# Performance work log

Measured on AMD Instinct MI355X. Metric: run time of the kernel, lower is better.

Reference implementation:

```python
import jax, jax.numpy as jnp
import numpy as np
import math

DIM = 147      # input feature dim
EMB = 64       # in_dim * head_cnt
M = 32         # int(EMB * kernel_ratio)
EPS_LN = 1e-5
EPS = 1e-8


def layer_norm(x, g, b, eps=EPS_LN):
    mu = jnp.mean(x, axis=-1, keepdims=True)
    var = jnp.mean(jnp.square(x - mu), axis=-1, keepdims=True)
    return (x - mu) * jax.lax.rsqrt(var + eps) * g + b


def prm_exp(x, W_rf):
    # x: [b, t, e], W_rf: [m, e]
    xd = 0.5 * jnp.sum(x * x, axis=-1, keepdims=True)        # [b, t, 1]
    wtx = jnp.einsum('bte,me->btm', x, W_rf)                  # [b, t, m]
    return jnp.exp(wtx - xd) / math.sqrt(M)


def setup_inputs() -> dict:
    key = jax.random.key(0)
    ks = jax.random.split(key, 16)
    B, T = 32, 3136
    s_in = 1.0 / math.sqrt(DIM)
    s_emb = 1.0 / math.sqrt(EMB)
    inp = {
        'x':      jax.random.normal(ks[0], (B, T, DIM), jnp.float32),
        'w_kqv':  jax.random.uniform(ks[1], (3 * EMB, DIM), jnp.float32, -s_in, s_in),
        'b_kqv':  jax.random.uniform(ks[2], (3 * EMB,), jnp.float32, -s_in, s_in),
        'w_proj': jax.random.uniform(ks[3], (EMB, EMB), jnp.float32, -s_emb, s_emb),
        'b_proj': jax.random.uniform(ks[4], (EMB,), jnp.float32, -s_emb, s_emb),
        'g1':     jnp.ones((DIM,), jnp.float32),
        'beta1':  jnp.zeros((DIM,), jnp.float32),
        'g2':     jnp.ones((EMB,), jnp.float32),
        'beta2':  jnp.zeros((EMB,), jnp.float32),
        'w_m1':   jax.random.uniform(ks[5], (EMB, EMB), jnp.float32, -s_emb, s_emb),
        'b_m1':   jax.random.uniform(ks[6], (EMB,), jnp.float32, -s_emb, s_emb),
        'w_m2':   jax.random.uniform(ks[7], (EMB, EMB), jnp.float32, -s_emb, s_emb),
        'b_m2':   jax.random.uniform(ks[8], (EMB,), jnp.float32, -s_emb, s_emb),
        # orthogonal random-feature matrix scaled by sqrt(m) (buffer 'w')
        'W_rf':   jnp.asarray(np.linalg.qr(np.random.RandomState(0).randn(EMB, EMB))[0][:M] * math.sqrt(M), jnp.float32),
    }
    return inp


def reference(x, w_kqv, b_kqv, w_proj, b_proj, g1, beta1, g2, beta2,
              w_m1, b_m1, w_m2, b_m2, W_rf):
    # --- single_attn(norm1(x)) ---
    xn = layer_norm(x, g1, beta1)
    kqv = xn @ w_kqv.T + b_kqv                                  # [b, t, 3e]
    k, q, v = jnp.split(kqv, 3, axis=-1)
    kp = prm_exp(k, W_rf)                                       # [b, t, m]
    qp = prm_exp(q, W_rf)                                       # [b, t, m]
    D = jnp.einsum('btm,bm->bt', qp, kp.sum(axis=1))[..., None]  # [b, t, 1]
    kptv = jnp.einsum('bte,btm->bem', v, kp)                    # [b, e, m]
    y = jnp.einsum('btm,bem->bte', qp, kptv) / (D + EPS)        # [b, t, e]
    y = v + (y @ w_proj.T + b_proj)                             # residual on v
    # --- y + mlp(norm2(y)) ---
    yn = layer_norm(y, g2, beta2)
    h = jax.nn.gelu(yn @ w_m1.T + b_m1, approximate=False)
    out = y + (h @ w_m2.T + b_m2)
    return out
```

## Files before the change

### kernel.cpp

```cpp
#include <hip/hip_runtime.h>
#include <hip/hip_bf16.h>

#define BB 32
#define TT 3136
#define DD 147
#define EE 64
#define MM 32
#define BT (BB*TT)

typedef __hip_bfloat16 bf16;
typedef __attribute__((ext_vector_type(8))) short s8v;
typedef __attribute__((ext_vector_type(4))) float f4v;

__device__ __forceinline__ float b2f(bf16 v){ return __bfloat162float(v); }
__device__ __forceinline__ bf16 f2b(float v){ return __float2bfloat16(v); }
__device__ __forceinline__ unsigned pack2(float a, float b){
  union { bf16 h[2]; unsigned u; } cv; cv.h[0]=f2b(a); cv.h[1]=f2b(b); return cv.u;
}

template<typename T>
__device__ __forceinline__ float cvt1(T v);
template<> __device__ __forceinline__ float cvt1<float>(float v){ return v; }
template<> __device__ __forceinline__ float cvt1<bf16>(bf16 v){ return __bfloat162float(v); }

__device__ __forceinline__ int bf16flag(const void* g1){
  return (*(const unsigned*)g1 == 0x3F803F80u) ? 1 : 0;
}

template<typename T>
__device__ void cvt_body(int idx,
    const T* wkqv, const T* bkqv, const T* Wrf, const T* wproj, const T* bproj,
    const T* g2, const T* be2, const T* wm1, const T* bm1, const T* wm2,
    const T* bm2, const T* g1, const T* be1,
    bf16* Bprep, bf16* WrfB, bf16* w0B, float* bprojF,
    float* g2F, float* be2F, bf16* w1B, float* bm1F, bf16* w2B,
    float* bm2F, float* c2F)
{
  if (idx < 30720){
    int n = idx/160, k = idx - n*160;
    Bprep[idx] = f2b(k < DD ? cvt1(wkqv[n*DD + k]) * cvt1(g1[k]) : 0.f);
    return;
  }
  idx -= 30720;
  if (idx < 2048){ WrfB[idx] = f2b(cvt1(Wrf[idx])); return; }
  idx -= 2048;
  if (idx < 4608){
    int e = idx/72, c = idx - e*72;
    w0B[idx] = f2b(c < 64 ? cvt1(wproj[e*64 + c]) : 0.f); return;
  }
  idx -= 4608;
  if (idx < 64){ bprojF[idx] = cvt1(bproj[idx]); return; }
  idx -= 64;
  if (idx < 64){ g2F[idx] = cvt1(g2[idx]); return; }
  idx -= 64;
  if (idx < 64){ be2F[idx] = cvt1(be2[idx]); return; }
  idx -= 64;
  if (idx < 4608){
    int e = idx/72, c = idx - e*72;
    w1B[idx] = f2b(c < 64 ? cvt1(wm1[e*64 + c]) : 0.f); return;
  }
  idx -= 4608;
  if (idx < 64){ bm1F[idx] = cvt1(bm1[idx]); return; }
  idx -= 64;
  if (idx < 4608){
    int e = idx/72, c = idx - e*72;
    w2B[idx] = f2b(c < 64 ? cvt1(wm2[e*64 + c]) : 0.f); return;
  }
  idx -= 4608;
  if (idx < 64){ bm2F[idx] = cvt1(bm2[idx]); return; }
  idx -= 64;
  if (idx < 12288){
    int n = idx>>6, ln = idx&63;
    float s = cvt1(wkqv[n*DD + ln])    * cvt1(be1[ln])
            + cvt1(wkqv[n*DD + 64+ln]) * cvt1(be1[64+ln]);
    if (ln < DD-128)
      s = fmaf(cvt1(wkqv[n*DD + 128+ln]), cvt1(be1[128+ln]), s);
    #pragma unroll
    for (int off=32; off; off>>=1) s += __shfl_xor(s, off);
    if (ln == 0) c2F[n] = s + cvt1(bkqv[n]);
    return;
  }
}

__global__ void k_cvt(const void* wkqv, const void* bkqv, const void* Wrf,
    const void* wproj, const void* bproj, const void* g2, const void* be2,
    const void* wm1, const void* bm1, const void* wm2, const void* bm2,
    const void* g1, const void* be1,
    bf16* Bprep, bf16* WrfB, bf16* w0B, float* bprojF,
    float* g2F, float* be2F, bf16* w1B, float* bm1F, bf16* w2B,
    float* bm2F, float* c2F)
{
  int idx = blockIdx.x*256 + threadIdx.x;
  if (bf16flag(g1))
    cvt_body<bf16>(idx, (const bf16*)wkqv, (const bf16*)bkqv, (const bf16*)Wrf,
      (const bf16*)wproj, (const bf16*)bproj, (const bf16*)g2, (const bf16*)be2,
      (const bf16*)wm1, (const bf16*)bm1, (const bf16*)wm2, (const bf16*)bm2,
      (const bf16*)g1, (const bf16*)be1,
      Bprep, WrfB, w0B, bprojF, g2F, be2F, w1B, bm1F, w2B, bm2F, c2F);
  else
    cvt_body<float>(idx, (const float*)wkqv, (const float*)bkqv, (const float*)Wrf,
      (const float*)wproj, (const float*)bproj, (const float*)g2, (const float*)be2,
      (const float*)wm1, (const float*)bm1, (const float*)wm2, (const float*)bm2,
      (const float*)g1, (const float*)be1,
      Bprep, WrfB, w0B, bprojF, g2F, be2F, w1B, bm1F, w2B, bm2F, c2F);
}

__global__ __launch_bounds__(256,4) void k_a2(
    const void* __restrict__ x, const void* __restrict__ g1,
    const bf16* __restrict__ Bprep, const float* __restrict__ c2F,
    const bf16* __restrict__ WrfB,
    bf16* __restrict__ qpG, bf16* __restrict__ vG,
    float* __restrict__ kptvP, float* __restrict__ ksumP)
{
  __shared__ __align__(16) char smem[21504];
  __shared__ float ksumW[128];
  bf16* vT   = (bf16*)smem;
  bf16* kpT  = (bf16*)(smem + 9216);
  bf16* qpT  = (bf16*)(smem + 13824);

  int tid = threadIdx.x;
  size_t t0 = (size_t)blockIdx.x*64;

  int tw = tid>>6, lane = tid&63, quad = lane>>4, r = lane&15;
  int tRow = tw*16 + quad*4;
  char* strip = smem + tw*5376;
  bf16* lin = (bf16*)strip;
  bf16* aS  = (bf16*)strip;
  bf16* kqW = (bf16*)strip;

  if (bf16flag(g1)){
    const uint4* xg = (const uint4*)((const bf16*)x + (t0 + (size_t)tw*16)*DD);
    uint4* xo = (uint4*)lin;
    #pragma unroll
    for (int k=0; k<5; ++k){
      int c = k*64 + lane;
      if (c < 294) xo[c] = xg[c];
    }
  } else {
    const float4* xg = (const float4*)((const float*)x + (t0 + (size_t)tw*16)*DD);
    uint2* xo = (uint2*)lin;
    #pragma unroll
    for (int k=0; k<10; ++k){
      int c = k*64 + lane;
      if (c < 588){
        float4 f = xg[c];
        uint2 u; u.x = pack2(f.x, f.y); u.y = pack2(f.z, f.w);
        xo[c] = u;
      }
    }
  }

  int ti = lane>>2, sl = lane&3;
  const bf16* srow = lin + ti*DD;
  float xv[37];
  float s1 = 0.f, s2 = 0.f;
  #pragma unroll
  for (int j=0; j<37; ++j){
    int e = sl + 4*j;
    float vx = (e < DD) ? b2f(srow[e]) : 0.f;
    xv[j] = vx;
    s1 += vx;
    s2 = fmaf(vx, vx, s2);
  }
  s1 += __shfl_xor(s1,1); s1 += __shfl_xor(s1,2);
  s2 += __shfl_xor(s2,1); s2 += __shfl_xor(s2,2);
  float mu  = s1 * (1.f/147.f);
  float var = s2 * (1.f/147.f) - mu*mu;
  float rn  = rsqrtf(var + 1e-5f);

  bf16* arow = aS + ti*168;
  #pragma unroll
  for (int j=0; j<37; ++j){
    int e = sl + 4*j;
    if (e < DD)       arow[e] = f2b((xv[j]-mu)*rn);
    else if (e == DD) arow[e] = f2b(0.f);
  }
  arow[148+sl] = f2b(0.f); arow[152+sl] = f2b(0.f); arow[156+sl] = f2b(0.f);

  f4v zero = {0.f,0.f,0.f,0.f};

  float c2v[12];
  #pragma unroll
  for (int nt=0; nt<12; ++nt) c2v[nt] = c2F[nt*16 + r];

  f4v acc[12];
  #pragma unroll
  for (int nt=0; nt<12; ++nt) acc[nt] = zero;
  const bf16* aBase = aS + r*168 + quad*8;
  const bf16* bBase = &Bprep[r*160 + quad*8];
  #pragma unroll
  for (int ks=0; ks<5; ++ks){
    s8v a = *((const s8v*)(aBase + ks*32));
    #pragma unroll
    for (int nt=0; nt<12; ++nt){
      s8v bw = *((const s8v*)(bBase + nt*16*160 + ks*32));
      acc[nt] = __builtin_amdgcn_mfma_f32_16x16x32_bf16(a, bw, acc[nt], 0,0,0);
    }
  }

  float vv[4][4];
  #pragma unroll
  for (int nt=8; nt<12; ++nt)
    #pragma unroll
    for (int reg=0; reg<4; ++reg)
      vv[nt-8][reg] = acc[nt][reg] + c2v[nt];

  float kq[8][4];
  #pragma unroll
  for (int nt=0; nt<8; ++nt)
    #pragma unroll
    for (int reg=0; reg<4; ++reg)
      kq[nt][reg] = acc[nt][reg] + c2v[nt];

  #pragma unroll
  for (int nt=0; nt<8; ++nt)
    #pragma unroll
    for (int reg=0; reg<4; ++reg)
      kqW[(quad*4+reg)*136 + nt*16 + r] = f2b(kq[nt][reg]);

  float xdk[4], xdq[4];
  #pragma unroll
  for (int reg=0; reg<4; ++reg){
    float sk = 0.f, sq = 0.f;
    #pragma unroll
    for (int nt=0; nt<4; ++nt){
      sk = fmaf(kq[nt][reg],   kq[nt][reg],   sk);
      sq = fmaf(kq[nt+4][reg], kq[nt+4][reg], sq);
    }
    #pragma unroll
    for (int off=1; off<16; off<<=1){
      sk += __shfl_xor(sk, off);
      sq += __shfl_xor(sq, off);
    }
    xdk[reg] = 0.5f*sk;
    xdq[reg] = 0.5f*sq;
  }

  f4v accP[2] = {zero, zero}, accQ[2] = {zero, zero};
  #pragma unroll
  for (int ks=0; ks<2; ++ks){
    s8v ak = *((const s8v*)&kqW[r*136 + ks*32 + quad*8]);
    s8v aq = *((const s8v*)&kqW[r*136 + 64 + ks*32 + quad*8]);
    #pragma unroll
    for (int nt=0; nt<2; ++nt){
      s8v wf = *((const s8v*)&WrfB[(nt*16+r)*64 + ks*32 + quad*8]);
      accP[nt] = __builtin_amdgcn_mfma_f32_16x16x32_bf16(ak, wf, accP[nt], 0,0,0);
      accQ[nt] = __builtin_amdgcn_mfma_f32_16x16x32_bf16(aq, wf, accQ[nt], 0,0,0);
    }
  }
  float kpv[2][4], qpv[2][4];
  #pragma unroll
  for (int nt=0; nt<2; ++nt){
    #pragma unroll
    for (int reg=0; reg<4; ++reg){
      kpv[nt][reg] = expf(accP[nt][reg] - xdk[reg]) * 0.17677669529663687f;
      qpv[nt][reg] = expf(accQ[nt][reg] - xdq[reg]) * 0.17677669529663687f;
    }
  }
  __syncthreads();

  #pragma unroll
  for (int nt=0; nt<4; ++nt){
    *((unsigned*)&vT[(nt*16+r)*72 + tRow])     = pack2(vv[nt][0], vv[nt][1]);
    *((unsigned*)&vT[(nt*16+r)*72 + tRow + 2]) = pack2(vv[nt][2], vv[nt][3]);
  }
  #pragma unroll
  for (int nt=0; nt<2; ++nt){
    *((unsigned*)&kpT[(nt*16+r)*72 + tRow])     = pack2(kpv[nt][0], kpv[nt][1]);
    *((unsigned*)&kpT[(nt*16+r)*72 + tRow + 2]) = pack2(kpv[nt][2], kpv[nt][3]);
    *((unsigned*)&qpT[(nt*16+r)*72 + tRow])     = pack2(qpv[nt][0], qpv[nt][1]);
    *((unsigned*)&qpT[(nt*16+r)*72 + tRow + 2]) = pack2(qpv[nt][2], qpv[nt][3]);
  }

  float ks0 = kpv[0][0]+kpv[0][1]+kpv[0][2]+kpv[0][3];
  float ks1 = kpv[1][0]+kpv[1][1]+kpv[1][2]+kpv[1][3];
  ks0 += __shfl_xor(ks0, 16); ks0 += __shfl_xor(ks0, 32);
  ks1 += __shfl_xor(ks1, 16); ks1 += __shfl_xor(ks1, 32);
  if (lane < 16){
    ksumW[tw*32 + r]      = ks0;
    ksumW[tw*32 + 16 + r] = ks1;
  }
  __syncthreads();

  {
    uint4* vg = (uint4*)(vG + (size_t)blockIdx.x*4096);
    for (int i=tid; i<512; i+=256){
      int e = i>>3, q = i&7;
      vg[i] = *((const uint4*)&vT[e*72 + q*8]);
    }
    uint4* qg = (uint4*)(qpG + (size_t)blockIdx.x*2048);
    {
      int m = tid>>3, q = tid&7;
      qg[tid] = *((const uint4*)&qpT[m*72 + q*8]);
    }
  }
  if (tid < 32)
    ksumP[(size_t)blockIdx.x*32 + tid] =
      ksumW[tid] + ksumW[32+tid] + ksumW[64+tid] + ksumW[96+tid];

  f4v accKV[2] = {zero, zero};
  #pragma unroll
  for (int kh=0; kh<2; ++kh){
    s8v av = *((const s8v*)&vT[(tw*16+r)*72 + kh*32 + quad*8]);
    #pragma unroll
    for (int nt=0; nt<2; ++nt){
      s8v bk = *((const s8v*)&kpT[(nt*16+r)*72 + kh*32 + quad*8]);
      accKV[nt] = __builtin_amdgcn_mfma_f32_16x16x32_bf16(av, bk, accKV[nt], 0,0,0);
    }
  }
  float* dst = kptvP + (size_t)blockIdx.x*2048;
  #pragma unroll
  for (int nt=0; nt<2; ++nt)
    #pragma unroll
    for (int reg=0; reg<4; ++reg)
      dst[(tw*16 + quad*4 + reg)*32 + nt*16 + r] = accKV[nt][reg];
}

__global__ void k_red(const float* __restrict__ kptvP,
                      const float* __restrict__ ksumP,
                      float* __restrict__ kptvF, float* __restrict__ ksumF){
  int idx = blockIdx.x*256 + threadIdx.x;
  if (idx < 65536){
    int b = idx >> 11, i = idx & 2047;
    const float* src = kptvP + (size_t)b*49*2048 + i;
    float s = 0.f;
    #pragma unroll 7
    for (int j=0; j<49; ++j) s += src[j*2048];
    kptvF[idx] = s;
  } else if (idx < 66560){
    int k = idx - 65536;
    int b = k >> 5, m = k & 31;
    const float* src = ksumP + (size_t)b*49*32 + m;
    float s = 0.f;
    #pragma unroll 7
    for (int j=0; j<49; ++j) s += src[j*32];
    ksumF[k] = s;
  }
}

__global__ __launch_bounds__(256,5) void k_b(
    const bf16* __restrict__ qpG, const bf16* __restrict__ vG,
    const float* __restrict__ kptvF, const float* __restrict__ ksumF,
    const bf16* __restrict__ w0B, const float* __restrict__ bprojF,
    const float* __restrict__ g2F, const float* __restrict__ be2F,
    const bf16* __restrict__ w1B, const float* __restrict__ bm1F,
    const bf16* __restrict__ w2B, const float* __restrict__ bm2F,
    const void* __restrict__ g1, void* __restrict__ outp)
{
  __shared__ __align__(16) bf16 qpS[64*40];
  __shared__ __align__(16) bf16 kvS[64*40];
  __shared__ __align__(16) bf16 vS[64*72];
  __shared__ __align__(16) bf16 stA[64*72];
  __shared__ float ksS[32];
  __shared__ float bpS[64], b1S[64], b2S[64], gS[64], btS[64];

  int flag = bf16flag(g1);
  int tid = threadIdx.x;
  int b = blockIdx.y;
  int gt0 = b*TT + blockIdx.x*64;
  int blk = b*49 + blockIdx.x;

  {
    int m = tid>>3, q = tid&7;
    union { uint4 u4; bf16 h[8]; } cv;
    cv.u4 = ((const uint4*)(qpG + (size_t)blk*2048))[tid];
    #pragma unroll
    for (int j=0; j<8; ++j)
      qpS[(q*8+j)*40 + m] = cv.h[j];
  }
  for (int i=tid; i<512; i+=256){
    int e = i>>3, q = i&7;
    float4 f = ((const float4*)(kptvF + b*2048))[i];
    union { bf16 h[4]; uint2 u; } cv;
    cv.h[0]=f2b(f.x); cv.h[1]=f2b(f.y); cv.h[2]=f2b(f.z); cv.h[3]=f2b(f.w);
    *((uint2*)&kvS[e*40 + q*4]) = cv.u;
  }
  for (int i=tid; i<512; i+=256){
    int e = i>>3, q = i&7;
    *((uint4*)&vS[e*72 + q*8]) = ((const uint4*)(vG + (size_t)blk*4096))[i];
  }
  if (tid<32) ksS[tid] = ksumF[b*32+tid];
  if (tid<64){
    bpS[tid]=bprojF[tid]; b1S[tid]=bm1F[tid]; b2S[tid]=bm2F[tid];
    gS[tid]=g2F[tid]; btS[tid]=be2F[tid];
  }
  __syncthreads();

  int tw = tid>>6, lane = tid&63, quad = lane>>4, r = lane&15;
  int tRow = tw*16 + quad*4;
  f4v zero = {0.f,0.f,0.f,0.f};

  float dpart;
  {
    int ti = lane>>2, sl = lane&3;
    const bf16* qrow = &qpS[(tw*16+ti)*40];
    float s = 0.f;
    #pragma unroll
    for (int m=0; m<8; ++m) s = fmaf(b2f(qrow[sl*8+m]), ksS[sl*8+m], s);
    s += __shfl_xor(s,1); s += __shfl_xor(s,2);
    dpart = s;
  }
  float Dinv[4];
  #pragma unroll
  for (int reg=0; reg<4; ++reg){
    float d = __shfl(dpart, (lane & 0x30) + 4*reg);
    Dinv[reg] = 1.f/(d + 1e-8f);
  }

  f4v accA[4];
  {
    s8v aq = *((const s8v*)&qpS[(tw*16+r)*40 + quad*8]);
    #pragma unroll
    for (int nt=0; nt<4; ++nt){
      s8v bk = *((const s8v*)&kvS[(nt*16+r)*40 + quad*8]);
      accA[nt] = __builtin_amdgcn_mfma_f32_16x16x32_bf16(aq, bk, zero, 0,0,0);
    }
  }

  #pragma unroll
  for (int nt=0; nt<4; ++nt)
    #pragma unroll
    for (int reg=0; reg<4; ++reg)
      stA[(tRow+reg)*72 + nt*16 + r] = f2b(accA[nt][reg]*Dinv[reg]);

  f4v accY[4] = {zero, zero, zero, zero};
  #pragma unroll
  for (int kh=0; kh<2; ++kh){
    s8v ay = *((const s8v*)&stA[(tw*16+r)*72 + kh*32 + quad*8]);
    #pragma unroll
    for (int nt=0; nt<4; ++nt){
      s8v bw = *((const s8v*)&w0B[(nt*16+r)*72 + kh*32 + quad*8]);
      accY[nt] = __builtin_amdgcn_mfma_f32_16x16x32_bf16(ay, bw, accY[nt], 0,0,0);
    }
  }
  float y[4][4];
  #pragma unroll
  for (int nt=0; nt<4; ++nt){
    int e = nt*16 + r;
    float bp = bpS[e];
    #pragma unroll
    for (int reg=0; reg<4; ++reg)
      y[nt][reg] = accY[nt][reg] + b2f(vS[e*72 + (tRow+reg)]) + bp;
  }

  float mu[4], rs[4];
  #pragma unroll
  for (int reg=0; reg<4; ++reg){
    float s = y[0][reg]+y[1][reg]+y[2][reg]+y[3][reg];
    #pragma unroll
    for (int off=1; off<16; off<<=1) s += __shfl_xor(s, off);
    mu[reg] = s * (1.f/64.f);
  }
  #pragma unroll
  for (int reg=0; reg<4; ++reg){
    float d2 = 0.f;
    #pragma unroll
    for (int nt=0; nt<4; ++nt){ float d = y[nt][reg]-mu[reg]; d2 = fmaf(d,d,d2); }
    #pragma unroll
    for (int off=1; off<16; off<<=1) d2 += __shfl_xor(d2, off);
    rs[reg] = rsqrtf(d2*(1.f/64.f) + 1e-5f);
  }
  #pragma unroll
  for (int nt=0; nt<4; ++nt){
    int e = nt*16 + r;
    float g = gS[e], be = btS[e];
    #pragma unroll
    for (int reg=0; reg<4; ++reg)
      stA[(tRow+reg)*72 + e] = f2b((y[nt][reg]-mu[reg])*rs[reg]*g + be);
  }

  f4v accH[4] = {zero, zero, zero, zero};
  #pragma unroll
  for (int kh=0; kh<2; ++kh){
    s8v ah = *((const s8v*)&stA[(tw*16+r)*72 + kh*32 + quad*8]);
    #pragma unroll
    for (int nt=0; nt<4; ++nt){
      s8v bw = *((const s8v*)&w1B[(nt*16+r)*72 + kh*32 + quad*8]);
      accH[nt] = __builtin_amdgcn_mfma_f32_16x16x32_bf16(ah, bw, accH[nt], 0,0,0);
    }
  }
  #pragma unroll
  for (int nt=0; nt<4; ++nt){
    int e = nt*16 + r;
    float b1 = b1S[e];
    #pragma unroll
    for (int reg=0; reg<4; ++reg){
      float h = accH[nt][reg] + b1;
      h = 0.5f*h*(1.f + erff(h*0.70710678118654752f));
      stA[(tRow+reg)*72 + e] = f2b(h);
    }
  }

  f4v accO[4] = {zero, zero, zero, zero};
  #pragma unroll
  for (int kh=0; kh<2; ++kh){
    s8v ao = *((const s8v*)&stA[(tw*16+r)*72 + kh*32 + quad*8]);
    #pragma unroll
    for (int nt=0; nt<4; ++nt){
      s8v bw = *((const s8v*)&w2B[(nt*16+r)*72 + kh*32 + quad*8]);
      accO[nt] = __builtin_amdgcn_mfma_f32_16x16x32_bf16(ao, bw, accO[nt], 0,0,0);
    }
  }
  if (flag){
    #pragma unroll
    for (int nt=0; nt<4; ++nt){
      int e = nt*16 + r;
      float b2 = b2S[e];
      #pragma unroll
      for (int reg=0; reg<4; ++reg)
        stA[(tRow+reg)*72 + e] = f2b(y[nt][reg] + accO[nt][reg] + b2);
    }
    __syncthreads();
    bf16* o = (bf16*)outp + (size_t)gt0*64;
    for (int i=tid; i<512; i+=256){
      int t = i>>3, q = i&7;
      *((uint4*)(o + t*64 + q*8)) = *((const uint4*)&stA[t*72 + q*8]);
    }
  } else {
    float* o = (float*)outp;
    #pragma unroll
    for (int nt=0; nt<4; ++nt){
      int e = nt*16 + r;
      float b2 = b2S[e];
      #pragma unroll
      for (int reg=0; reg<4; ++reg)
        o[(size_t)(gt0 + tRow + reg)*64 + e] = y[nt][reg] + accO[nt][reg] + b2;
    }
  }
}

extern "C" void kernel_launch(void* const* d_in, const int* in_sizes, int n_in,
                              void* d_out, int out_size, void* d_ws, size_t ws_size,
                              hipStream_t stream){
  const void* x    = d_in[0];
  const void* wkqv = d_in[1];
  const void* bkqv = d_in[2];
  const void* wproj= d_in[3];
  const void* bproj= d_in[4];
  const void* g1   = d_in[5];
  const void* be1  = d_in[6];
  const void* g2   = d_in[7];
  const void* be2  = d_in[8];
  const void* wm1  = d_in[9];
  const void* bm1  = d_in[10];
  const void* wm2  = d_in[11];
  const void* bm2  = d_in[12];
  const void* Wrf  = d_in[13];

  char* ws = (char*)d_ws;
  bf16*  Bprep = (bf16*) (ws + 256);
  bf16*  WrfB  = (bf16*) (ws + 62464);
  bf16*  w0B   = (bf16*) (ws + 66560);
  float* bprojF= (float*)(ws + 82944);
  float* g2F   = (float*)(ws + 83200);
  float* be2F  = (float*)(ws + 83456);
  bf16*  w1B   = (bf16*) (ws + 83712);
  float* bm1F  = (float*)(ws + 100096);
  bf16*  w2B   = (bf16*) (ws + 100352);
  float* bm2F  = (float*)(ws + 116736);
  float* c2F   = (float*)(ws + 118784);
  float* kptvP = (float*)(ws + 131072);
  float* ksumP = (float*)(ws + 12976128);
  float* kptvF = (float*)(ws + 32231424);
  float* ksumF = (float*)(ws + 32493568);
  bf16*  qpG   = (bf16*) (ws + 32497664);
  bf16*  vG    = (bf16*) (ws + 38920192);

  k_cvt<<<256, 256, 0, stream>>>(wkqv, bkqv, Wrf, wproj, bproj, g2, be2,
      wm1, bm1, wm2, bm2, g1, be1,
      Bprep, WrfB, w0B, bprojF, g2F, be2F, w1B, bm1F, w2B, bm2F, c2F);
  k_a2<<<BT/64, 256, 0, stream>>>(x, g1, Bprep, c2F, WrfB,
      qpG, vG, kptvP, ksumP);
  k_red<<<260, 256, 0, stream>>>(kptvP, ksumP, kptvF, ksumF);
  k_b<<<dim3(TT/64, BB), 256, 0, stream>>>(qpG, vG, kptvF, ksumF,
      w0B, bprojF, g2F, be2F, w1B, bm1F, w2B, bm2F, g1, d_out);
}
```

Measured before the change: 178.3 us.

## Process two token tiles per block in k_a2 and prefetch the second tile

Each k_a2 block now handles two consecutive 64-token tiles in a loop, and the grid is halved. On the bf16-input path the second tile's x rows are loaded into registers while the first tile is computed, to hide global load latency. On the fp32 path there is no prefetch, so the change only halves the block count and serialises work within each block. It adds register pressure from the prefetch buffer and an extra barrier between tiles.

```diff
diff --git a/kernel.cpp b/kernel.cpp
--- a/kernel.cpp
+++ b/kernel.cpp
@@ -119,201 +119,224 @@
   bf16* qpT  = (bf16*)(smem + 13824);
 
   int tid = threadIdx.x;
-  size_t t0 = (size_t)blockIdx.x*64;
-
   int tw = tid>>6, lane = tid&63, quad = lane>>4, r = lane&15;
   int tRow = tw*16 + quad*4;
   char* strip = smem + tw*5376;
   bf16* lin = (bf16*)strip;
   bf16* aS  = (bf16*)strip;
   bf16* kqW = (bf16*)strip;
-
-  if (bf16flag(g1)){
-    const uint4* xg = (const uint4*)((const bf16*)x + (t0 + (size_t)tw*16)*DD);
-    uint4* xo = (uint4*)lin;
-    #pragma unroll
-    for (int k=0; k<5; ++k){
-      int c = k*64 + lane;
-      if (c < 294) xo[c] = xg[c];
-    }
-  } else {
-    const float4* xg = (const float4*)((const float*)x + (t0 + (size_t)tw*16)*DD);
-    uint2* xo = (uint2*)lin;
-    #pragma unroll
-    for (int k=0; k<10; ++k){
-      int c = k*64 + lane;
-      if (c < 588){
-        float4 f = xg[c];
-        uint2 u; u.x = pack2(f.x, f.y); u.y = pack2(f.z, f.w);
-        xo[c] = u;
-      }
-    }
-  }
-
-  int ti = lane>>2, sl = lane&3;
-  const bf16* srow = lin + ti*DD;
-  float xv[37];
-  float s1 = 0.f, s2 = 0.f;
-  #pragma unroll
-  for (int j=0; j<37; ++j){
-    int e = sl + 4*j;
-    float vx = (e < DD) ? b2f(srow[e]) : 0.f;
-    xv[j] = vx;
-    s1 += vx;
-    s2 = fmaf(vx, vx, s2);
-  }
-  s1 += __shfl_xor(s1,1); s1 += __shfl_xor(s1,2);
-  s2 += __shfl_xor(s2,1); s2 += __shfl_xor(s2,2);
-  float mu  = s1 * (1.f/147.f);
-  float var = s2 * (1.f/147.f) - mu*mu;
-  float rn  = rsqrtf(var + 1e-5f);
-
-  bf16* arow = aS + ti*168;
-  #pragma unroll
-  for (int j=0; j<37; ++j){
-    int e = sl + 4*j;
-    if (e < DD)       arow[e] = f2b((xv[j]-mu)*rn);
-    else if (e == DD) arow[e] = f2b(0.f);
-  }
-  arow[148+sl] = f2b(0.f); arow[152+sl] = f2b(0.f); arow[156+sl] = f2b(0.f);
-
-  f4v zero = {0.f,0.f,0.f,0.f};
-
-  float c2v[12];
-  #pragma unroll
-  for (int nt=0; nt<12; ++nt) c2v[nt] = c2F[nt*16 + r];
-
-  f4v acc[12];
-  #pragma unroll
-  for (int nt=0; nt<12; ++nt) acc[nt] = zero;
-  const bf16* aBase = aS + r*168 + quad*8;
-  const bf16* bBase = &Bprep[r*160 + quad*8];
-  #pragma unroll
-  for (int ks=0; ks<5; ++ks){
-    s8v a = *((const s8v*)(aBase + ks*32));
-    #pragma unroll
-    for (int nt=0; nt<12; ++nt){
-      s8v bw = *((const s8v*)(bBase + nt*16*160 + ks*32));
-      acc[nt] = __builtin_amdgcn_mfma_f32_16x16x32_bf16(a, bw, acc[nt], 0,0,0);
-    }
-  }
-
-  float vv[4][4];
-  #pragma unroll
-  for (int nt=8; nt<12; ++nt)
-    #pragma unroll
-    for (int reg=0; reg<4; ++reg)
-      vv[nt-8][reg] = acc[nt][reg] + c2v[nt];
-
-  float kq[8][4];
-  #pragma unroll
-  for (int nt=0; nt<8; ++nt)
-    #pragma unroll
-    for (int reg=0; reg<4; ++reg)
-      kq[nt][reg] = acc[nt][reg] + c2v[nt];
-
-  #pragma unroll
-  for (int nt=0; nt<8; ++nt)
-    #pragma unroll
-    for (int reg=0; reg<4; ++reg)
-      kqW[(quad*4+reg)*136 + nt*16 + r] = f2b(kq[nt][reg]);
-
-  float xdk[4], xdq[4];
-  #pragma unroll
-  for (int reg=0; reg<4; ++reg){
-    float sk = 0.f, sq = 0.f;
+  int flag = bf16flag(g1);
+
+  uint4 pf[5];
+
+  for (int tt=0; tt<2; ++tt){
+    size_t tileId = (size_t)blockIdx.x*2 + tt;
+    size_t t0 = tileId*64;
+
+    if (flag){
+      if (tt == 0){
+        const uint4* xg  = (const uint4*)((const bf16*)x + (t0 + (size_t)tw*16)*DD);
+        const uint4* xg1 = (const uint4*)((const bf16*)x + (t0 + 64 + (size_t)tw*16)*DD);
+        uint4* xo = (uint4*)lin;
+        #pragma unroll
+        for (int k=0; k<5; ++k){
+          int c = k*64 + lane;
+          if (c < 294) xo[c] = xg[c];
+        }
+        #pragma unroll
+        for (int k=0; k<5; ++k){
+          int c = k*64 + lane;
+          pf[k] = (c < 294) ? xg1[c] : make_uint4(0u,0u,0u,0u);
+        }
+      } else {
+        uint4* xo = (uint4*)lin;
+        #pragma unroll
+        for (int k=0; k<5; ++k){
+          int c = k*64 + lane;
+          if (c < 294) xo[c] = pf[k];
+        }
+      }
+    } else {
+      const float4* xg = (const float4*)((const float*)x + (t0 + (size_t)tw*16)*DD);
+      uint2* xo = (uint2*)lin;
+      #pragma unroll
+      for (int k=0; k<10; ++k){
+        int c = k*64 + lane;
+        if (c < 588){
+          float4 f = xg[c];
+          uint2 u; u.x = pack2(f.x, f.y); u.y = pack2(f.z, f.w);
+          xo[c] = u;
+        }
+      }
+    }
+
+    int ti = lane>>2, sl = lane&3;
+    const bf16* srow = lin + ti*DD;
+    float xv[37];
+    float s1 = 0.f, s2 = 0.f;
+    #pragma unroll
+    for (int j=0; j<37; ++j){
+      int e = sl + 4*j;
+      float vx = (e < DD) ? b2f(srow[e]) : 0.f;
+      xv[j] = vx;
+      s1 += vx;
+      s2 = fmaf(vx, vx, s2);
+    }
+    s1 += __shfl_xor(s1,1); s1 += __shfl_xor(s1,2);
+    s2 += __shfl_xor(s2,1); s2 += __shfl_xor(s2,2);
+    float mu  = s1 * (1.f/147.f);
+    float var = s2 * (1.f/147.f) - mu*mu;
+    float rn  = rsqrtf(var + 1e-5f);
+
+    bf16* arow = aS + ti*168;
+    #pragma unroll
+    for (int j=0; j<37; ++j){
+      int e = sl + 4*j;
+      if (e < DD)       arow[e] = f2b((xv[j]-mu)*rn);
+      else if (e == DD) arow[e] = f2b(0.f);
+    }
+    arow[148+sl] = f2b(0.f); arow[152+sl] = f2b(0.f); arow[156+sl] = f2b(0.f);
+
+    f4v zero = {0.f,0.f,0.f,0.f};
+
+    float c2v[12];
+    #pragma unroll
+    for (int nt=0; nt<12; ++nt) c2v[nt] = c2F[nt*16 + r];
+
+    f4v acc[12];
+    #pragma unroll
+    for (int nt=0; nt<12; ++nt) acc[nt] = zero;
+    const bf16* aBase = aS + r*168 + quad*8;
+    const bf16* bBase = &Bprep[r*160 + quad*8];
+    #pragma unroll
+    for (int ks=0; ks<5; ++ks){
+      s8v a = *((const s8v*)(aBase + ks*32));
+      #pragma unroll
+      for (int nt=0; nt<12; ++nt){
+        s8v bw = *((const s8v*)(bBase + nt*16*160 + ks*32));
+        acc[nt] = __builtin_amdgcn_mfma_f32_16x16x32_bf16(a, bw, acc[nt], 0,0,0);
+      }
+    }
+
+    float vv[4][4];
+    #pragma unroll
+    for (int nt=8; nt<12; ++nt)
+      #pragma unroll
+      for (int reg=0; reg<4; ++reg)
+        vv[nt-8][reg] = acc[nt][reg] + c2v[nt];
+
+    float kq[8][4];
+    #pragma unroll
+    for (int nt=0; nt<8; ++nt)
+      #pragma unroll
+      for (int reg=0; reg<4; ++reg)
+        kq[nt][reg] = acc[nt][reg] + c2v[nt];
+
+    #pragma unroll
+    for (int nt=0; nt<8; ++nt)
+      #pragma unroll
+      for (int reg=0; reg<4; ++reg)
+        kqW[(quad*4+reg)*136 + nt*16 + r] = f2b(kq[nt][reg]);
+
+    float xdk[4], xdq[4];
+    #pragma unroll
+    for (int reg=0; reg<4; ++reg){
+      float sk = 0.f, sq = 0.f;
+      #pragma unroll
+      for (int nt=0; nt<4; ++nt){
+        sk = fmaf(kq[nt][reg],   kq[nt][reg],   sk);
+        sq = fmaf(kq[nt+4][reg], kq[nt+4][reg], sq);
+      }
+      #pragma unroll
+      for (int off=1; off<16; off<<=1){
+        sk += __shfl_xor(sk, off);
+        sq += __shfl_xor(sq, off);
+      }
+      xdk[reg] = 0.5f*sk;
+      xdq[reg] = 0.5f*sq;
+    }
+
+    f4v accP[2] = {zero, zero}, accQ[2] = {zero, zero};
+    #pragma unroll
+    for (int ks=0; ks<2; ++ks){
+      s8v ak = *((const s8v*)&kqW[r*136 + ks*32 + quad*8]);
+      s8v aq = *((const s8v*)&kqW[r*136 + 64 + ks*32 + quad*8]);
+      #pragma unroll
+      for (int nt=0; nt<2; ++nt){
+        s8v wf = *((const s8v*)&WrfB[(nt*16+r)*64 + ks*32 + quad*8]);
+        accP[nt] = __builtin_amdgcn_mfma_f32_16x16x32_bf16(ak, wf, accP[nt], 0,0,0);
+        accQ[nt] = __builtin_amdgcn_mfma_f32_16x16x32_bf16(aq, wf, accQ[nt], 0,0,0);
+      }
+    }
+    float kpv[2][4], qpv[2][4];
+    #pragma unroll
+    for (int nt=0; nt<2; ++nt){
+      #pragma unroll
+      for (int reg=0; reg<4; ++reg){
+        kpv[nt][reg] = expf(accP[nt][reg] - xdk[reg]) * 0.17677669529663687f;
+        qpv[nt][reg] = expf(accQ[nt][reg] - xdq[reg]) * 0.17677669529663687f;
+      }
+    }
+    __syncthreads();
+
     #pragma unroll
     for (int nt=0; nt<4; ++nt){
-      sk = fmaf(kq[nt][reg],   kq[nt][reg],   sk);
-      sq = fmaf(kq[nt+4][reg], kq[nt+4][reg], sq);
-    }
-    #pragma unroll
-    for (int off=1; off<16; off<<=1){
-      sk += __shfl_xor(sk, off);
-      sq += __shfl_xor(sq, off);
-    }
-    xdk[reg] = 0.5f*sk;
-    xdq[reg] = 0.5f*sq;
-  }
-
-  f4v accP[2] = {zero, zero}, accQ[2] = {zero, zero};
-  #pragma unroll
-  for (int ks=0; ks<2; ++ks){
-    s8v ak = *((const s8v*)&kqW[r*136 + ks*32 + quad*8]);
-    s8v aq = *((const s8v*)&kqW[r*136 + 64 + ks*32 + quad*8]);
+      *((unsigned*)&vT[(nt*16+r)*72 + tRow])     = pack2(vv[nt][0], vv[nt][1]);
+      *((unsigned*)&vT[(nt*16+r)*72 + tRow + 2]) = pack2(vv[nt][2], vv[nt][3]);
+    }
     #pragma unroll
     for (int nt=0; nt<2; ++nt){
-      s8v wf = *((const s8v*)&WrfB[(nt*16+r)*64 + ks*32 + quad*8]);
-      accP[nt] = __builtin_amdgcn_mfma_f32_16x16x32_bf16(ak, wf, accP[nt], 0,0,0);
-      accQ[nt] = __builtin_amdgcn_mfma_f32_16x16x32_bf16(aq, wf, accQ[nt], 0,0,0);
-    }
-  }
-  float kpv[2][4], qpv[2][4];
-  #pragma unroll
-  for (int nt=0; nt<2; ++nt){
-    #pragma unroll
-    for (int reg=0; reg<4; ++reg){
-      kpv[nt][reg] = expf(accP[nt][reg] - xdk[reg]) * 0.17677669529663687f;
-      qpv[nt][reg] = expf(accQ[nt][reg] - xdq[reg]) * 0.17677669529663687f;
-    }
-  }
-  __syncthreads();
-
-  #pragma unroll
-  for (int nt=0; nt<4; ++nt){
-    *((unsigned*)&vT[(nt*16+r)*72 + tRow])     = pack2(vv[nt][0], vv[nt][1]);
-    *((unsigned*)&vT[(nt*16+r)*72 + tRow + 2]) = pack2(vv[nt][2], vv[nt][3]);
-  }
-  #pragma unroll
-  for (int nt=0; nt<2; ++nt){
-    *((unsigned*)&kpT[(nt*16+r)*72 + tRow])     = pack2(kpv[nt][0], kpv[nt][1]);
-    *((unsigned*)&kpT[(nt*16+r)*72 + tRow + 2]) = pack2(kpv[nt][2], kpv[nt][3]);
-    *((unsigned*)&qpT[(nt*16+r)*72 + tRow])     = pack2(qpv[nt][0], qpv[nt][1]);
-    *((unsigned*)&qpT[(nt*16+r)*72 + tRow + 2]) = pack2(qpv[nt][2], qpv[nt][3]);
-  }
-
-  float ks0 = kpv[0][0]+kpv[0][1]+kpv[0][2]+kpv[0][3];
-  float ks1 = kpv[1][0]+kpv[1][1]+kpv[1][2]+kpv[1][3];
-  ks0 += __shfl_xor(ks0, 16); ks0 += __shfl_xor(ks0, 32);
-  ks1 += __shfl_xor(ks1, 16); ks1 += __shfl_xor(ks1, 32);
-  if (lane < 16){
-    ksumW[tw*32 + r]      = ks0;
-    ksumW[tw*32 + 16 + r] = ks1;
-  }
-  __syncthreads();
-
-  {
-    uint4* vg = (uint4*)(vG + (size_t)blockIdx.x*4096);
-    for (int i=tid; i<512; i+=256){
-      int e = i>>3, q = i&7;
-      vg[i] = *((const uint4*)&vT[e*72 + q*8]);
-    }
-    uint4* qg = (uint4*)(qpG + (size_t)blockIdx.x*2048);
+      *((unsigned*)&kpT[(nt*16+r)*72 + tRow])     = pack2(kpv[nt][0], kpv[nt][1]);
+      *((unsigned*)&kpT[(nt*16+r)*72 + tRow + 2]) = pack2(kpv[nt][2], kpv[nt][3]);
+      *((unsigned*)&qpT[(nt*16+r)*72 + tRow])     = pack2(qpv[nt][0], qpv[nt][1]);
+      *((unsigned*)&qpT[(nt*16+r)*72 + tRow + 2]) = pack2(qpv[nt][2], qpv[nt][3]);
+    }
+
+    float ks0 = kpv[0][0]+kpv[0][1]+kpv[0][2]+kpv[0][3];
+    float ks1 = kpv[1][0]+kpv[1][1]+kpv[1][2]+kpv[1][3];
+    ks0 += __shfl_xor(ks0, 16); ks0 += __shfl_xor(ks0, 32);
+    ks1 += __shfl_xor(ks1, 16); ks1 += __shfl_xor(ks1, 32);
+    if (lane < 16){
+      ksumW[tw*32 + r]      = ks0;
+      ksumW[tw*32 + 16 + r] = ks1;
+    }
+    __syncthreads();
+
     {
-      int m = tid>>3, q = tid&7;
-      qg[tid] = *((const uint4*)&qpT[m*72 + q*8]);
-    }
-  }
-  if (tid < 32)
-    ksumP[(size_t)blockIdx.x*32 + tid] =
-      ksumW[tid] + ksumW[32+tid] + ksumW[64+tid] + ksumW[96+tid];
-
-  f4v accKV[2] = {zero, zero};
-  #pragma unroll
-  for (int kh=0; kh<2; ++kh){
-    s8v av = *((const s8v*)&vT[(tw*16+r)*72 + kh*32 + quad*8]);
-    #pragma unroll
-    for (int nt=0; nt<2; ++nt){
-      s8v bk = *((const s8v*)&kpT[(nt*16+r)*72 + kh*32 + quad*8]);
-      accKV[nt] = __builtin_amdgcn_mfma_f32_16x16x32_bf16(av, bk, accKV[nt], 0,0,0);
-    }
-  }
-  float* dst = kptvP + (size_t)blockIdx.x*2048;
-  #pragma unroll
-  for (int nt=0; nt<2; ++nt)
-    #pragma unroll
-    for (int reg=0; reg<4; ++reg)
-      dst[(tw*16 + quad*4 + reg)*32 + nt*16 + r] = accKV[nt][reg];
+      uint4* vg = (uint4*)(vG + tileId*4096);
+      for (int i=tid; i<512; i+=256){
+        int e = i>>3, q = i&7;
+        vg[i] = *((const uint4*)&vT[e*72 + q*8]);
+      }
+      uint4* qg = (uint4*)(qpG + tileId*2048);
+      {
+        int m = tid>>3, q = tid&7;
+        qg[tid] = *((const uint4*)&qpT[m*72 + q*8]);
+      }
+    }
+    if (tid < 32)
+      ksumP[tileId*32 + tid] =
+        ksumW[tid] + ksumW[32+tid] + ksumW[64+tid] + ksumW[96+tid];
+
+    f4v accKV[2] = {zero, zero};
+    #pragma unroll
+    for (int kh=0; kh<2; ++kh){
+      s8v av = *((const s8v*)&vT[(tw*16+r)*72 + kh*32 + quad*8]);
+      #pragma unroll
+      for (int nt=0; nt<2; ++nt){
+        s8v bk = *((const s8v*)&kpT[(nt*16+r)*72 + kh*32 + quad*8]);
+        accKV[nt] = __builtin_amdgcn_mfma_f32_16x16x32_bf16(av, bk, accKV[nt], 0,0,0);
+      }
+    }
+    float* dst = kptvP + tileId*2048;
+    #pragma unroll
+    for (int nt=0; nt<2; ++nt)
+      #pragma unroll
+      for (int reg=0; reg<4; ++reg)
+        dst[(tw*16 + quad*4 + reg)*32 + nt*16 + r] = accKV[nt][reg];
+
+    if (tt == 0) __syncthreads();
+  }
 }
 
 __global__ void k_red(const float* __restrict__ kptvP,
@@ -569,7 +592,7 @@
   k_cvt<<<256, 256, 0, stream>>>(wkqv, bkqv, Wrf, wproj, bproj, g2, be2,
       wm1, bm1, wm2, bm2, g1, be1,
       Bprep, WrfB, w0B, bprojF, g2F, be2F, w1B, bm1F, w2B, bm2F, c2F);
-  k_a2<<<BT/64, 256, 0, stream>>>(x, g1, Bprep, c2F, WrfB,
+  k_a2<<<BT/128, 256, 0, stream>>>(x, g1, Bprep, c2F, WrfB,
       qpG, vG, kptvP, ksumP);
   k_red<<<260, 256, 0, stream>>>(kptvP, ksumP, kptvF, ksumF);
   k_b<<<dim3(TT/64, BB), 256, 0, stream>>>(qpG, vG, kptvF, ksumF,
```

Measured after the change: 334.7 us. 1.88x slower.
